# Performance work log

Hardware: AMD Instinct MI355X
Metric: run time of the kernel (lower is better)

## Reference

```python
import jax, jax.numpy as jnp
import numpy as np

K = 3
STRIDE = 1
PAD = 1
DIL = 1


def _conv2d(x, w, b, stride, pad):
    y = jax.lax.conv_general_dilated(
        x, w, (stride, stride), [(pad, pad), (pad, pad)],
        dimension_numbers=('NCHW', 'OIHW', 'NCHW'))
    return y + b[None, :, None, None]


def setup_inputs() -> dict:
    key = jax.random.key(0)
    ks = jax.random.split(key, 6)
    N, Cin, Cout, H, W = 4, 64, 64, 128, 128
    x = jax.random.normal(ks[0], (N, Cin, H, W), jnp.float32)
    w_off = jax.random.normal(ks[1], (2 * K * K, Cin, K, K), jnp.float32) * 0.01
    b_off = jnp.zeros((2 * K * K,), jnp.float32)
    w_mask = jax.random.normal(ks[2], (K * K, Cin, K, K), jnp.float32) * 0.01
    b_mask = jnp.zeros((K * K,), jnp.float32)
    weight = jax.random.normal(ks[3], (Cout, Cin, K, K), jnp.float32) * 0.05
    bias = jax.random.normal(ks[4], (Cout,), jnp.float32)
    return {"x": x, "w_off": w_off, "b_off": b_off,
            "w_mask": w_mask, "b_mask": b_mask,
            "weight": weight, "bias": bias}


def _deform_conv(x, offset, weight, bias):
    # x: [N,C,H,W]; offset: [N,2*K2,Ho,Wo] with channel layout (dy,dx) per kernel pt
    N, C, H, W = x.shape
    K2 = K * K
    Ho, Wo = offset.shape[2], offset.shape[3]
    off_y = offset[:, 0::2]  # [N,K2,Ho,Wo]
    off_x = offset[:, 1::2]
    ki = jnp.arange(K2) // K
    kj = jnp.arange(K2) % K
    base_y = (jnp.arange(Ho) * STRIDE - PAD)[None, :, None] + (ki * DIL)[:, None, None]
    base_x = (jnp.arange(Wo) * STRIDE - PAD)[None, None, :] + (kj * DIL)[:, None, None]
    py = base_y[None].astype(off_y.dtype) + off_y  # [N,K2,Ho,Wo]
    px = base_x[None].astype(off_x.dtype) + off_x
    y0 = jnp.floor(py)
    x0 = jnp.floor(px)
    wy = py - y0
    wx = px - x0
    xf = x.reshape(N, C, H * W)

    def corner(yi, xi):
        valid = (yi >= 0) & (yi <= H - 1) & (xi >= 0) & (xi <= W - 1)
        yc = jnp.clip(yi, 0, H - 1).astype(jnp.int32)
        xc = jnp.clip(xi, 0, W - 1).astype(jnp.int32)
        idx = (yc * W + xc).reshape(N, -1)  # [N, K2*Ho*Wo]
        g = jnp.take_along_axis(xf, idx[:, None, :], axis=2)  # [N,C,K2*Ho*Wo]
        g = g.reshape(N, C, K2, Ho, Wo)
        return g * valid[:, None].astype(x.dtype)

    # bilinear interpolation with zero padding outside the image
    val = ((1 - wy) * (1 - wx))[:, None] * corner(y0, x0) \
        + ((1 - wy) * wx)[:, None] * corner(y0, x0 + 1) \
        + (wy * (1 - wx))[:, None] * corner(y0 + 1, x0) \
        + (wy * wx)[:, None] * corner(y0 + 1, x0 + 1)  # [N,C,K2,Ho,Wo]
    out = jnp.einsum('nckhw,ock->nohw', val,
                     weight.reshape(weight.shape[0], C, K2))
    return out + bias[None, :, None, None]


def reference(x, w_off, b_off, w_mask, b_mask, weight, bias):
    offset = _conv2d(x, w_off, b_off, STRIDE, PAD)              # [N,2*K2,Ho,Wo]
    mask = jax.nn.sigmoid(_conv2d(x, w_mask, b_mask, STRIDE, PAD))  # [N,K2,Ho,Wo]
    # source does mask.repeat(1,2,1,1) then offset*mask, then plain deform_conv2d
    offset = offset * jnp.concatenate([mask, mask], axis=1)
    return _deform_conv(x, offset, weight, bias)
```

## Files before the change

### kernel.cpp

```cpp
#include <hip/hip_runtime.h>
#include <math.h>

#define HD 128
#define WD 128
#define WP 130
#define CIN 64
#define COUT 64
#define NB 4
#define K2 9
#define HW (HD*WD)
#define CK 576
#define TP 32
#define TPF 16
#define NKK 18

#define WAM   (4 * NKK * 64 * 8)
#define WAO   (2 * NKK * 64 * 8)
#define XTP   ((size_t)NB * WP * WP * CIN)
#define OFFSZ ((size_t)NB * K2 * HW)
#define WTSZ  ((size_t)CK * COUT)

#define PRE_T 1024
#define PRE_H 65
#define PRE_P ((WAM + WAO) / 256)
#define HALO_PER_N 33024
#define HALO_W8 16512

typedef __attribute__((ext_vector_type(8))) short short8;
typedef __attribute__((ext_vector_type(4))) float f32x4;

__device__ inline unsigned short f2bf(float v) {
    unsigned int u = __float_as_uint(v);
    unsigned int r = u + 0x7fffu + ((u >> 16) & 1u);
    return (unsigned short)(r >> 16);
}
__device__ inline float bf2f(unsigned short b) {
    return __uint_as_float(((unsigned int)b) << 16);
}
__device__ inline unsigned int pack_bf16(float a, float b) {
#if __has_builtin(__builtin_amdgcn_cvt_pk_bf16_f32)
    auto r = __builtin_amdgcn_cvt_pk_bf16_f32(a, b);
    unsigned int u; __builtin_memcpy(&u, &r, 4); return u;
#else
    return ((unsigned int)f2bf(b) << 16) | (unsigned int)f2bf(a);
#endif
}
__device__ inline float2 up2(unsigned int u) {
    float2 r;
    r.x = __uint_as_float(u << 16);
    r.y = __uint_as_float(u & 0xffff0000u);
    return r;
}

__global__ __launch_bounds__(256) void pre_kernel(
    const float* __restrict__ x,
    const float* __restrict__ weight,
    const float* __restrict__ w_off,
    const float* __restrict__ w_mask,
    unsigned short* __restrict__ xp,
    short* __restrict__ mhi, short* __restrict__ ohi)
{
    __shared__ float tile[64][66];
    int bid = blockIdx.x;
    int t = threadIdx.x;

    if (bid < PRE_T) {
        int half = bid & 1;
        int h = (bid >> 1) & 127;
        int n = bid >> 8;
        int w0 = half * 64;
        int g = t >> 6, wl = t & 63;
        const float* xb = x + ((size_t)n * CIN) * HW + h * WD + w0;
        #pragma unroll
        for (int i = 0; i < 16; i++) {
            int cc = i * 4 + g;
            tile[wl][cc] = xb[(size_t)cc * HW + wl];
        }
        __syncthreads();
        size_t rowbase = (((size_t)n * WP + (h + 1)) * WP + (w0 + 1)) * CIN;
        #pragma unroll
        for (int i = 0; i < 8; i++) {
            int u = i * 256 + t;
            int ww = u >> 5;
            int cp = (u & 31) * 2;
            float2 v = *(const float2*)&tile[ww][cp];
            *(unsigned int*)&xp[rowbase + (size_t)ww * CIN + cp] = pack_bf16(v.x, v.y);
        }
    } else if (bid < PRE_T + PRE_H) {
        int widx = (bid - PRE_T) * 256 + t;
        if (widx < HALO_W8) {
            int s = widx * 8;
            int n = s / HALO_PER_N;
            int v = s - n * HALO_PER_N;
            size_t nb = (size_t)n * WP * WP * CIN;
            size_t base;
            if (v < 8320) {
                base = nb + v;
            } else if (v < 16640) {
                base = nb + (size_t)129 * WP * CIN + (v - 8320);
            } else if (v < 24832) {
                int v2 = v - 16640; int h = 1 + (v2 >> 6); int c = v2 & 63;
                base = nb + (size_t)h * WP * CIN + c;
            } else {
                int v3 = v - 24832; int h = 1 + (v3 >> 6); int c = v3 & 63;
                base = nb + ((size_t)h * WP + 129) * CIN + c;
            }
            short8 z = {0, 0, 0, 0, 0, 0, 0, 0};
            *(short8*)&xp[base] = z;
        }
    } else {
        int gid = (bid - PRE_T - PRE_H) * 256 + t;
        if (gid < WAM) {
            int idx = gid;
            int jj = idx & 7;
            int lane = (idx >> 3) & 63;
            int kk = (idx >> 9) % NKK;
            int mt = (idx >> 9) / NKK;
            int o = mt * 16 + (lane & 15);
            int rp = kk * 32 + (lane >> 4) * 8 + jj;
            int k = rp >> 6, c = rp & 63;
            mhi[idx] = (short)f2bf(weight[((size_t)o * CIN + c) * 9 + k]);
        } else {
            int idx = gid - WAM;
            int jj = idx & 7;
            int lane = (idx >> 3) & 63;
            int kk = (idx >> 9) % NKK;
            int mt = (idx >> 9) / NKK;
            int j = mt * 16 + (lane & 15);
            int rp = kk * 32 + (lane >> 4) * 8 + jj;
            int k = rp >> 6, c = rp & 63;
            float w = 0.f;
            if (j < 18)      w = w_off[((size_t)j * CIN + c) * 9 + k];
            else if (j < 27) w = w_mask[((size_t)(j - 18) * CIN + c) * 9 + k];
            ohi[idx] = (short)f2bf(w);
        }
    }
}

__global__ __launch_bounds__(256, 3) void fused_kernel(
    const unsigned short* __restrict__ xp,
    const short* __restrict__ waM_hi,
    const short* __restrict__ waO_hi,
    const float* __restrict__ b_off, const float* __restrict__ b_mask,
    const float* __restrict__ bias,
    float* __restrict__ out)
{
    __shared__ __align__(16) short val_hi[72 * 256];
    __shared__ float conv_s[27 * 32];
    __shared__ float4 p_w4[K2 * TP];
    __shared__ int4   p_idx4[K2 * TP];

    int t = threadIdx.x;
    int wv = t >> 6;
    int lane = t & 63;
    int wo0 = blockIdx.x * TP;
    int ho  = blockIdx.y;
    int n   = blockIdx.z;
    const unsigned short* xpn = xp + (size_t)n * WP * WP * CIN;
    int p16 = lane & 15, quad = lane >> 4;

    #pragma unroll
    for (int i = 0; i < 9; i++) {
        int u = t + 256 * i;
        int tap = u >> 8;
        int p = (u >> 3) & 31;
        int g = u & 7;
        int ti = tap / 3, tj = tap - ti * 3;
        const short8 v = *(const short8*)&xpn[((size_t)(ho + ti) * WP + (wo0 + p + tj)) * CIN + g * 8];
        int c2 = tap * 8 + g;
        *(short8*)&val_hi[c2 * 256 + ((p + c2) & 31) * 8] = v;
    }
    __syncthreads();

    {
        int jt = wv >> 1, pt = wv & 1;
        f32x4 acc = {0.f, 0.f, 0.f, 0.f};
        #pragma unroll
        for (int kk = 0; kk < NKK; kk++) {
            int abase = ((jt * NKK + kk) * 64 + lane) * 8;
            short8 ah = *(const short8*)&waO_hi[abase];
            int c2 = kk * 4 + quad;
            short8 b = *(const short8*)&val_hi[c2 * 256 + ((pt * 16 + p16 + c2) & 31) * 8];
            acc = __builtin_amdgcn_mfma_f32_16x16x32_bf16(ah, b, acc, 0, 0, 0);
        }
        #pragma unroll
        for (int i = 0; i < 4; i++) {
            int j = jt * 16 + quad * 4 + i;
            if (j < 27) {
                float bv = (j < 18) ? b_off[j] : b_mask[j - 18];
                conv_s[j * 32 + pt * 16 + p16] = acc[i] + bv;
            }
        }
    }
    __syncthreads();

    #pragma unroll
    for (int pass = 0; pass < 2; pass++) {
        int u = t + pass * 256;
        if (u < K2 * TP) {
            int k = u >> 5, p = u & 31;
            float oy_raw = conv_s[(2 * k) * 32 + p];
            float ox_raw = conv_s[(2 * k + 1) * 32 + p];
            float my = 1.f / (1.f + expf(-conv_s[(18 + (2 * k) % 9) * 32 + p]));
            float mx = 1.f / (1.f + expf(-conv_s[(18 + (2 * k + 1) % 9) * 32 + p]));
            float oy = oy_raw * my;
            float ox = ox_raw * mx;
            int ki = k / 3, kj = k - ki * 3;
            int wo = wo0 + p;
            float py = (float)(ho - 1 + ki) + oy;
            float px = (float)(wo - 1 + kj) + ox;
            float y0f = floorf(py), x0f = floorf(px);
            float wy = py - y0f, wx = px - x0f;
            int y0 = (int)y0f, x0 = (int)x0f;
            float wy0 = 1.f - wy, wx0 = 1.f - wx;
            int y0c = min(max(y0, 0), HD - 1);
            int y1c = min(max(y0 + 1, 0), HD - 1);
            int x0c = min(max(x0, 0), WD - 1);
            int x1c = min(max(x0 + 1, 0), WD - 1);
            bool vy0 = (y0 >= 0) && (y0 < HD);
            bool vy1 = (y0 + 1 >= 0) && (y0 + 1 < HD);
            bool vx0 = (x0 >= 0) && (x0 < WD);
            bool vx1 = (x0 + 1 >= 0) && (x0 + 1 < WD);
            float4 w4;
            w4.x = (vy0 && vx0) ? wy0 * wx0 : 0.f;
            w4.y = (vy0 && vx1) ? wy0 * wx  : 0.f;
            w4.z = (vy1 && vx0) ? wy  * wx0 : 0.f;
            w4.w = (vy1 && vx1) ? wy  * wx  : 0.f;
            int4 i4;
            i4.x = ((y0c + 1) * WP + (x0c + 1)) * CIN;
            i4.y = ((y0c + 1) * WP + (x1c + 1)) * CIN;
            i4.z = ((y1c + 1) * WP + (x0c + 1)) * CIN;
            i4.w = ((y1c + 1) * WP + (x1c + 1)) * CIN;
            p_w4[u] = w4;
            p_idx4[u] = i4;
        }
    }
    __syncthreads();

    #pragma unroll
    for (int i = 0; i < 9; i++) {
        int u = t + 256 * i;
        int task = u >> 3;
        int g = u & 7;
        int c0 = g * 8;
        int k = task >> 5, p = task & 31;
        float4 w4 = p_w4[task];
        int4  i4 = p_idx4[task];
        uint4 qa = *(const uint4*)&xpn[i4.x + c0];
        uint4 qb = *(const uint4*)&xpn[i4.y + c0];
        uint4 qc = *(const uint4*)&xpn[i4.z + c0];
        uint4 qd = *(const uint4*)&xpn[i4.w + c0];
        unsigned int qa_[4] = {qa.x, qa.y, qa.z, qa.w};
        unsigned int qb_[4] = {qb.x, qb.y, qb.z, qb.w};
        unsigned int qc_[4] = {qc.x, qc.y, qc.z, qc.w};
        unsigned int qd_[4] = {qd.x, qd.y, qd.z, qd.w};
        unsigned int r_[4];
        #pragma unroll
        for (int d = 0; d < 4; d++) {
            float2 fa = up2(qa_[d]), fb = up2(qb_[d]), fc = up2(qc_[d]), fd = up2(qd_[d]);
            float2 gg;
            gg.x = w4.x * fa.x + w4.y * fb.x + w4.z * fc.x + w4.w * fd.x;
            gg.y = w4.x * fa.y + w4.y * fb.y + w4.z * fc.y + w4.w * fd.y;
            r_[d] = pack_bf16(gg.x, gg.y);
        }
        uint4 r = {r_[0], r_[1], r_[2], r_[3]};
        int c2 = k * 8 + g;
        *(uint4*)&val_hi[c2 * 256 + ((p + c2) & 31) * 8] = r;
    }
    __syncthreads();

    f32x4 a0 = {0.f, 0.f, 0.f, 0.f};
    f32x4 a1 = {0.f, 0.f, 0.f, 0.f};
    #pragma unroll
    for (int kk = 0; kk < NKK; kk++) {
        int abase = ((wv * NKK + kk) * 64 + lane) * 8;
        short8 ah = *(const short8*)&waM_hi[abase];
        int c2 = kk * 4 + quad;
        short8 b0 = *(const short8*)&val_hi[c2 * 256 + ((p16 + c2) & 31) * 8];
        short8 b1 = *(const short8*)&val_hi[c2 * 256 + ((16 + p16 + c2) & 31) * 8];
        a0 = __builtin_amdgcn_mfma_f32_16x16x32_bf16(ah, b0, a0, 0, 0, 0);
        a1 = __builtin_amdgcn_mfma_f32_16x16x32_bf16(ah, b1, a1, 0, 0, 0);
    }

    size_t obase = ((size_t)n * COUT) * HW + (size_t)ho * WD + wo0;
    #pragma unroll
    for (int i = 0; i < 4; i++) {
        int o = wv * 16 + quad * 4 + i;
        float bv = bias[o];
        out[obase + (size_t)o * HW + p16] = a0[i] + bv;
        out[obase + (size_t)o * HW + 16 + p16] = a1[i] + bv;
    }
}

__global__ void transpose_w_kernel(const float* __restrict__ w, float* __restrict__ wt) {
    int i = blockIdx.x * 256 + threadIdx.x;
    int o = i / CK;
    int ck = i - o * CK;
    wt[ck * COUT + o] = w[i];
}

__global__ __launch_bounds__(256) void offmask_kernel(
    const float* __restrict__ x,
    const float* __restrict__ w_off, const float* __restrict__ b_off,
    const float* __restrict__ w_mask, const float* __restrict__ b_mask,
    float* __restrict__ offy, float* __restrict__ offx)
{
    __shared__ float ws[CK][27];
    int t = threadIdx.x;
    for (int i = t; i < CK * 27; i += 256) {
        int j = i % 27;
        int citap = i / 27;
        int ci = citap / 9;
        int tap = citap - ci * 9;
        float v;
        if (j < 18) v = w_off[(j * CIN + ci) * 9 + tap];
        else        v = w_mask[((j - 18) * CIN + ci) * 9 + tap];
        ws[citap][j] = v;
    }
    __syncthreads();

    int pix = blockIdx.x * 256 + t;
    int n  = pix >> 14;
    int ho = (pix >> 7) & 127;
    int wo = pix & 127;

    float acc[27];
    #pragma unroll
    for (int j = 0; j < 18; j++) acc[j] = b_off[j];
    #pragma unroll
    for (int j = 0; j < 9; j++)  acc[18 + j] = b_mask[j];

    int offs[9];
    bool oks[9];
    #pragma unroll
    for (int dy = 0; dy < 3; dy++) {
        int y = ho - 1 + dy;
        #pragma unroll
        for (int dx = 0; dx < 3; dx++) {
            int xx = wo - 1 + dx;
            bool ok = (y >= 0) && (y < HD) && (xx >= 0) && (xx < WD);
            oks[dy * 3 + dx] = ok;
            offs[dy * 3 + dx] = (ok ? y : 0) * WD + (ok ? xx : 0);
        }
    }
    const float* xn = x + (size_t)n * CIN * HW;
    for (int ci = 0; ci < CIN; ci++) {
        const float* xc = xn + (size_t)ci * HW;
        float v[9];
        #pragma unroll
        for (int tap = 0; tap < 9; tap++)
            v[tap] = oks[tap] ? xc[offs[tap]] : 0.f;
        #pragma unroll
        for (int tap = 0; tap < 9; tap++) {
            const float* wrow = ws[ci * 9 + tap];
            float vv = v[tap];
            #pragma unroll
            for (int j = 0; j < 27; j++) acc[j] += wrow[j] * vv;
        }
    }
    float m[9];
    #pragma unroll
    for (int j = 0; j < 9; j++) m[j] = 1.f / (1.f + expf(-acc[18 + j]));
    #pragma unroll
    for (int k = 0; k < 9; k++) {
        int cy = 2 * k, cx = 2 * k + 1;
        float my = m[cy < 9 ? cy : cy - 9];
        float mx = m[cx < 9 ? cx : cx - 9];
        size_t o = (((size_t)n * K2 + k) * HD + ho) * WD + wo;
        offy[o] = acc[cy] * my;
        offx[o] = acc[cx] * mx;
    }
}

__global__ __launch_bounds__(256) void deform_kernel(
    const float* __restrict__ x,
    const float* __restrict__ offy, const float* __restrict__ offx,
    const float* __restrict__ wt,
    const float* __restrict__ bias,
    float* __restrict__ out)
{
    __shared__ __align__(16) float val_s[CK * TPF];
    __shared__ float4 p_w4[K2 * TPF];
    __shared__ int4   p_idx4[K2 * TPF];

    int t = threadIdx.x;
    int wo0 = blockIdx.x * TPF;
    int ho  = blockIdx.y;
    int n   = blockIdx.z;

    if (t < K2 * TPF) {
        int k = t >> 4, p = t & 15;
        int wo = wo0 + p;
        size_t oi = (((size_t)n * K2 + k) * HD + ho) * WD + wo;
        float oy = offy[oi], ox = offx[oi];
        int ki = k / 3, kj = k - ki * 3;
        float py = (float)(ho - 1 + ki) + oy;
        float px = (float)(wo - 1 + kj) + ox;
        float y0f = floorf(py), x0f = floorf(px);
        float wy = py - y0f, wx = px - x0f;
        int y0 = (int)y0f, x0 = (int)x0f;
        float wy0 = 1.f - wy, wx0 = 1.f - wx;
        int y0c = min(max(y0, 0), HD - 1);
        int y1c = min(max(y0 + 1, 0), HD - 1);
        int x0c = min(max(x0, 0), WD - 1);
        int x1c = min(max(x0 + 1, 0), WD - 1);
        bool vy0 = (y0 >= 0) && (y0 < HD);
        bool vy1 = (y0 + 1 >= 0) && (y0 + 1 < HD);
        bool vx0 = (x0 >= 0) && (x0 < WD);
        bool vx1 = (x0 + 1 >= 0) && (x0 + 1 < WD);
        float4 w4;
        w4.x = (vy0 && vx0) ? wy0 * wx0 : 0.f;
        w4.y = (vy0 && vx1) ? wy0 * wx  : 0.f;
        w4.z = (vy1 && vx0) ? wy  * wx0 : 0.f;
        w4.w = (vy1 && vx1) ? wy  * wx  : 0.f;
        int4 i4;
        i4.x = y0c * WD + x0c;
        i4.y = y0c * WD + x1c;
        i4.z = y1c * WD + x0c;
        i4.w = y1c * WD + x1c;
        p_w4[t] = w4;
        p_idx4[t] = i4;
    }
    __syncthreads();

    const float* xn = x + (size_t)n * CIN * HW;
    for (int e = t; e < CK * TPF; e += 256) {
        int row = e >> 4, p = e & 15;
        int cc = row / 9, k = row - cc * 9;
        int task = (k << 4) | p;
        float4 w4 = p_w4[task];
        int4  i4 = p_idx4[task];
        const float* xc = xn + (size_t)cc * HW;
        val_s[e] = w4.x * xc[i4.x] + w4.y * xc[i4.y]
                 + w4.z * xc[i4.z] + w4.w * xc[i4.w];
    }
    __syncthreads();

    int o = t & 63, q = t >> 6;
    float4 acc = {0.f, 0.f, 0.f, 0.f};
    const float4* v4 = (const float4*)val_s;
    const float* wp = wt + o;
    #pragma unroll 4
    for (int r = 0; r < CK; r++) {
        float w = wp[r * COUT];
        float4 vv = v4[r * 4 + q];
        acc.x += w * vv.x; acc.y += w * vv.y;
        acc.z += w * vv.z; acc.w += w * vv.w;
    }
    float b = bias[o];
    acc.x += b; acc.y += b; acc.z += b; acc.w += b;
    __syncthreads();
    float4* o4 = (float4*)val_s;
    o4[o * 4 + q] = acc;
    __syncthreads();
    size_t obase = ((size_t)n * COUT) * HW + (size_t)ho * WD + wo0;
    #pragma unroll
    for (int i = 0; i < 4; i++) {
        int l = t + 256 * i;
        int oo = l >> 4, p = l & 15;
        out[obase + (size_t)oo * HW + p] = val_s[l];
    }
}

extern "C" void kernel_launch(void* const* d_in, const int* in_sizes, int n_in,
                              void* d_out, int out_size, void* d_ws, size_t ws_size,
                              hipStream_t stream) {
    const float* x      = (const float*)d_in[0];
    const float* w_off  = (const float*)d_in[1];
    const float* b_off  = (const float*)d_in[2];
    const float* w_mask = (const float*)d_in[3];
    const float* b_mask = (const float*)d_in[4];
    const float* weight = (const float*)d_in[5];
    const float* bias   = (const float*)d_in[6];
    float* out = (float*)d_out;

    short* base = (short*)d_ws;
    short* waM_hi = base;
    short* waO_hi = waM_hi + WAM;
    unsigned short* xp = (unsigned short*)(waO_hi + WAO);
    size_t need = ((size_t)WAM + WAO + XTP) * sizeof(short);

    if (ws_size >= need) {
        pre_kernel<<<PRE_T + PRE_H + PRE_P, 256, 0, stream>>>(
            x, weight, w_off, w_mask, xp, waM_hi, waO_hi);
        fused_kernel<<<dim3(WD / TP, HD, NB), 256, 0, stream>>>(
            xp, waM_hi, waO_hi, b_off, b_mask, bias, out);
    } else {
        float* offy = (float*)d_ws;
        float* offx = offy + OFFSZ;
        float* wt   = offx + OFFSZ;
        transpose_w_kernel<<<144, 256, 0, stream>>>(weight, wt);
        offmask_kernel<<<256, 256, 0, stream>>>(x, w_off, b_off, w_mask, b_mask, offy, offx);
        deform_kernel<<<dim3(WD / TPF, HD, NB), 256, 0, stream>>>(x, offy, offx, wt, bias, out);
    }
}
```

Measured before the change: 113.2 us.

## Split sampled-value LDS buffer into two phases and read conv input directly from global

The offset/mask convolution now loads its B operands straight from global memory instead of staging the 3x3 neighbourhood in LDS. The bilinear sampling and main MFMA GEMM are split into two halves (taps 0-4, then 5-8) that reuse a smaller 40x256 LDS buffer. This cuts shared memory per block so launch bounds can rise from 3 to 4 blocks per CU. The cost is an extra barrier round and uncached, less coalesced global reads for the offset conv.

```diff
diff --git a/kernel.cpp b/kernel.cpp
--- a/kernel.cpp
+++ b/kernel.cpp
@@ -137,7 +137,7 @@
     }
 }
 
-__global__ __launch_bounds__(256, 3) void fused_kernel(
+__global__ __launch_bounds__(256, 4) void fused_kernel(
     const unsigned short* __restrict__ xp,
     const short* __restrict__ waM_hi,
     const short* __restrict__ waO_hi,
@@ -145,7 +145,7 @@
     const float* __restrict__ bias,
     float* __restrict__ out)
 {
-    __shared__ __align__(16) short val_hi[72 * 256];
+    __shared__ __align__(16) short val_s[40 * 256];
     __shared__ float conv_s[27 * 32];
     __shared__ float4 p_w4[K2 * TP];
     __shared__ int4   p_idx4[K2 * TP];
@@ -159,28 +159,19 @@
     const unsigned short* xpn = xp + (size_t)n * WP * WP * CIN;
     int p16 = lane & 15, quad = lane >> 4;
 
-    #pragma unroll
-    for (int i = 0; i < 9; i++) {
-        int u = t + 256 * i;
-        int tap = u >> 8;
-        int p = (u >> 3) & 31;
-        int g = u & 7;
-        int ti = tap / 3, tj = tap - ti * 3;
-        const short8 v = *(const short8*)&xpn[((size_t)(ho + ti) * WP + (wo0 + p + tj)) * CIN + g * 8];
-        int c2 = tap * 8 + g;
-        *(short8*)&val_hi[c2 * 256 + ((p + c2) & 31) * 8] = v;
-    }
-    __syncthreads();
-
     {
         int jt = wv >> 1, pt = wv & 1;
+        int p = pt * 16 + p16;
         f32x4 acc = {0.f, 0.f, 0.f, 0.f};
         #pragma unroll
         for (int kk = 0; kk < NKK; kk++) {
             int abase = ((jt * NKK + kk) * 64 + lane) * 8;
             short8 ah = *(const short8*)&waO_hi[abase];
-            int c2 = kk * 4 + quad;
-            short8 b = *(const short8*)&val_hi[c2 * 256 + ((pt * 16 + p16 + c2) & 31) * 8];
+            const int tap = kk >> 1;
+            const int ti = tap / 3;
+            const int tj = tap - ti * 3;
+            int g = (kk & 1) * 4 + quad;
+            const short8 b = *(const short8*)&xpn[((size_t)(ho + ti) * WP + (wo0 + p + tj)) * CIN + g * 8];
             acc = __builtin_amdgcn_mfma_f32_16x16x32_bf16(ah, b, acc, 0, 0, 0);
         }
         #pragma unroll
@@ -237,8 +228,11 @@
     }
     __syncthreads();
 
-    #pragma unroll
-    for (int i = 0; i < 9; i++) {
+    f32x4 a0 = {0.f, 0.f, 0.f, 0.f};
+    f32x4 a1 = {0.f, 0.f, 0.f, 0.f};
+
+    #pragma unroll
+    for (int i = 0; i < 5; i++) {
         int u = t + 256 * i;
         int task = u >> 3;
         int g = u & 7;
@@ -264,20 +258,62 @@
             r_[d] = pack_bf16(gg.x, gg.y);
         }
         uint4 r = {r_[0], r_[1], r_[2], r_[3]};
-        int c2 = k * 8 + g;
-        *(uint4*)&val_hi[c2 * 256 + ((p + c2) & 31) * 8] = r;
-    }
-    __syncthreads();
-
-    f32x4 a0 = {0.f, 0.f, 0.f, 0.f};
-    f32x4 a1 = {0.f, 0.f, 0.f, 0.f};
-    #pragma unroll
-    for (int kk = 0; kk < NKK; kk++) {
+        int c2b = k * 8 + g;
+        *(uint4*)&val_s[c2b * 256 + ((p + c2b) & 31) * 8] = r;
+    }
+    __syncthreads();
+
+    #pragma unroll
+    for (int kk = 0; kk < 10; kk++) {
         int abase = ((wv * NKK + kk) * 64 + lane) * 8;
         short8 ah = *(const short8*)&waM_hi[abase];
-        int c2 = kk * 4 + quad;
-        short8 b0 = *(const short8*)&val_hi[c2 * 256 + ((p16 + c2) & 31) * 8];
-        short8 b1 = *(const short8*)&val_hi[c2 * 256 + ((16 + p16 + c2) & 31) * 8];
+        int c2b = kk * 4 + quad;
+        short8 b0 = *(const short8*)&val_s[c2b * 256 + ((p16 + c2b) & 31) * 8];
+        short8 b1 = *(const short8*)&val_s[c2b * 256 + ((16 + p16 + c2b) & 31) * 8];
+        a0 = __builtin_amdgcn_mfma_f32_16x16x32_bf16(ah, b0, a0, 0, 0, 0);
+        a1 = __builtin_amdgcn_mfma_f32_16x16x32_bf16(ah, b1, a1, 0, 0, 0);
+    }
+    __syncthreads();
+
+    #pragma unroll
+    for (int i = 0; i < 4; i++) {
+        int u = t + 256 * i;
+        int task = u >> 3;
+        int g = u & 7;
+        int c0 = g * 8;
+        int kloc = task >> 5, p = task & 31;
+        float4 w4 = p_w4[160 + task];
+        int4  i4 = p_idx4[160 + task];
+        uint4 qa = *(const uint4*)&xpn[i4.x + c0];
+        uint4 qb = *(const uint4*)&xpn[i4.y + c0];
+        uint4 qc = *(const uint4*)&xpn[i4.z + c0];
+        uint4 qd = *(const uint4*)&xpn[i4.w + c0];
+        unsigned int qa_[4] = {qa.x, qa.y, qa.z, qa.w};
+        unsigned int qb_[4] = {qb.x, qb.y, qb.z, qb.w};
+        unsigned int qc_[4] = {qc.x, qc.y, qc.z, qc.w};
+        unsigned int qd_[4] = {qd.x, qd.y, qd.z, qd.w};
+        unsigned int r_[4];
+        #pragma unroll
+        for (int d = 0; d < 4; d++) {
+            float2 fa = up2(qa_[d]), fb = up2(qb_[d]), fc = up2(qc_[d]), fd = up2(qd_[d]);
+            float2 gg;
+            gg.x = w4.x * fa.x + w4.y * fb.x + w4.z * fc.x + w4.w * fd.x;
+            gg.y = w4.x * fa.y + w4.y * fb.y + w4.z * fc.y + w4.w * fd.y;
+            r_[d] = pack_bf16(gg.x, gg.y);
+        }
+        uint4 r = {r_[0], r_[1], r_[2], r_[3]};
+        int c2b = kloc * 8 + g;
+        *(uint4*)&val_s[c2b * 256 + ((p + c2b) & 31) * 8] = r;
+    }
+    __syncthreads();
+
+    #pragma unroll
+    for (int kk = 10; kk < NKK; kk++) {
+        int abase = ((wv * NKK + kk) * 64 + lane) * 8;
+        short8 ah = *(const short8*)&waM_hi[abase];
+        int c2b = kk * 4 + quad - 40;
+        short8 b0 = *(const short8*)&val_s[c2b * 256 + ((p16 + c2b) & 31) * 8];
+        short8 b1 = *(const short8*)&val_s[c2b * 256 + ((16 + p16 + c2b) & 31) * 8];
         a0 = __builtin_amdgcn_mfma_f32_16x16x32_bf16(ah, b0, a0, 0, 0, 0);
         a1 = __builtin_amdgcn_mfma_f32_16x16x32_bf16(ah, b1, a1, 0, 0, 0);
     }
```

Result: slower. 130.1 us (+14.9%).
